# Kernel optimization log

Measured on AMD Instinct MI355X. Metric: run time of the kernel, lower is better.

The kernel has to match this reference:

```python
import jax, jax.numpy as jnp
import numpy as np

B, C, D, H, W = 2, 64, 8, 32, 32
QK = max(1, C // 8)  # intermediate dim for query/key 1x1x1 convs


def setup_inputs() -> dict:
    key = jax.random.key(0)
    ks = jax.random.split(key, 8)
    s = 0.05
    return {
        "x": jax.random.normal(ks[0], (B, C, D, H, W), dtype=jnp.float32),
        "Wq": jax.random.normal(ks[1], (QK, C), dtype=jnp.float32) * s,
        "bq": jax.random.normal(ks[2], (QK,), dtype=jnp.float32) * s,
        "Wk": jax.random.normal(ks[3], (QK, C), dtype=jnp.float32) * s,
        "bk": jax.random.normal(ks[4], (QK,), dtype=jnp.float32) * s,
        "Wv": jax.random.normal(ks[5], (C, C), dtype=jnp.float32) * s,
        "bv": jax.random.normal(ks[6], (C,), dtype=jnp.float32) * s,
        "gamma": jax.random.normal(ks[7], (1,), dtype=jnp.float32) * s,
    }


def reference(x, Wq, bq, Wk, bk, Wv, bv, gamma):
    b, c, d, h, w = x.shape
    n = d * h * w
    xf = x.reshape(b, c, n)  # (B, C, N)
    # 1x1x1 convs == per-position linear maps over channels
    q = jnp.einsum('oc,bcn->bon', Wq, xf) + bq[None, :, None]  # (B, QK, N)
    k = jnp.einsum('oc,bcn->bon', Wk, xf) + bk[None, :, None]  # (B, QK, N)
    v = jnp.einsum('oc,bcn->bon', Wv, xf) + bv[None, :, None]  # (B, C,  N)
    # energy[b, i, j] = q[b, :, i] . k[b, :, j]
    energy = jnp.einsum('bqi,bqj->bij', q, k)  # (B, N, N)
    attn = jax.nn.softmax(energy, axis=-1)
    # out[b, c, i] = sum_j v[b, c, j] * attn[b, i, j]
    out = jnp.einsum('bcj,bij->bci', v, attn)  # (B, C, N)
    out = out.reshape(b, c, d, h, w)
    return gamma[0] * out + x
```

## Files before the change

kernel.cpp:

```cpp
#include <hip/hip_runtime.h>


using f32x16 = __attribute__((ext_vector_type(16))) float;
using u32x4  = __attribute__((ext_vector_type(4))) unsigned int;

#define LOG2E 1.4426950408889634f

static __device__ __forceinline__ f32x16 mfma_z(u32x4 a, u32x4 b) {
  f32x16 d;
  asm("v_mfma_f32_32x32x16_bf16 %0, %1, %2, 0" : "=v"(d) : "v"(a), "v"(b));
  return d;
}
static __device__ __forceinline__ void mfma_acc(f32x16& d, u32x4 a, u32x4 b) {
  asm("v_mfma_f32_32x32x16_bf16 %0, %1, %2, %0" : "+v"(d) : "v"(a), "v"(b));
}
static __device__ __forceinline__ unsigned pkbf(float lo, float hi) {
  unsigned r;
  asm("v_cvt_pk_bf16_f32 %0, %1, %2" : "=v"(r) : "v"(lo), "v"(hi));
  return r;
}
static __device__ __forceinline__ void plswap(unsigned& a, unsigned& b) {
  asm("v_permlane32_swap_b32 %0, %1" : "+v"(a), "+v"(b));
}
static __device__ __forceinline__ unsigned f2bf(float f) {
  union { float f; unsigned u; } v; v.f = f;
  return (v.u + 0x7fffu + ((v.u >> 16) & 1u)) >> 16;
}
static __device__ __forceinline__ u32x4 pack8(const float* p) {
  u32x4 r;
  r[0] = f2bf(p[0]) | (f2bf(p[1]) << 16);
  r[1] = f2bf(p[2]) | (f2bf(p[3]) << 16);
  r[2] = f2bf(p[4]) | (f2bf(p[5]) << 16);
  r[3] = f2bf(p[6]) | (f2bf(p[7]) << 16);
  return r;
}

__global__ __launch_bounds__(128) void k_proj_qk(
    const float* __restrict__ x, const float* __restrict__ Wq, const float* __restrict__ bq,
    const float* __restrict__ Wk, const float* __restrict__ bk,
    u32x4* __restrict__ Qf, u32x4* __restrict__ Kf) {
  __shared__ float sW[2][8][64];
  __shared__ float sb[2][8];
  const int tid = threadIdx.x;
  {
    float* w = &sW[0][0][0];
    for (int i = tid; i < 512; i += 128) { w[i] = Wq[i]; w[512 + i] = Wk[i]; }
    if (tid < 8) { sb[0][tid] = bq[tid]; sb[1][tid] = bk[tid]; }
  }
  __syncthreads();
  const int b    = blockIdx.x >> 7;
  const int nb   = blockIdx.x & 127;
  const int lane = tid & 63;
  const int wv   = tid >> 6;
  const int ql   = lane & 31, ch = lane >> 5;
  const int n    = nb * 64 + wv * 32 + ql;
  const float* xp = x + ((size_t)b << 19) + n;
  float aq[8], ak[8];
  #pragma unroll
  for (int o = 0; o < 8; ++o) { aq[o] = 0.f; ak[o] = 0.f; }
  #pragma unroll
  for (int ci = 0; ci < 32; ci += 4) {
    const int c = ch * 32 + ci;
    float xv[4];
    #pragma unroll
    for (int j = 0; j < 4; ++j) xv[j] = xp[(size_t)(c + j) << 13];
    #pragma unroll
    for (int o = 0; o < 8; ++o) {
      const float4 wq = *(const float4*)&sW[0][o][c];
      const float4 wk = *(const float4*)&sW[1][o][c];
      aq[o] += wq.x * xv[0] + wq.y * xv[1] + wq.z * xv[2] + wq.w * xv[3];
      ak[o] += wk.x * xv[0] + wk.y * xv[1] + wk.z * xv[2] + wk.w * xv[3];
    }
  }
  #pragma unroll
  for (int o = 0; o < 8; ++o) {
    aq[o] += __shfl_xor(aq[o], 32, 64);
    ak[o] += __shfl_xor(ak[o], 32, 64);
  }
  if (ch == 0) {
    float q8[8], k8[8];
    #pragma unroll
    for (int o = 0; o < 8; ++o) {
      q8[o] = (aq[o] + sb[0][o]) * LOG2E;
      k8[o] = ak[o] + sb[1][o];
    }
    Qf[((size_t)b << 13) + n] = pack8(q8);
    Kf[((size_t)b << 13) + n] = pack8(k8);
  }
}

__global__ __launch_bounds__(128) void k_proj_v(
    const float* __restrict__ x, const float* __restrict__ Wv, const float* __restrict__ bv,
    u32x4* __restrict__ Vf) {
  const int bid = blockIdx.x;
  const int b   = bid >> 7;
  const int coq = (bid >> 3) & 15;
  const int ngc = bid & 7;
  const int ng  = ngc * 128 + threadIdx.x;
  const int co  = coq * 4;
  float acc[4][8];
  #pragma unroll
  for (int i = 0; i < 4; ++i)
    #pragma unroll
    for (int e = 0; e < 8; ++e) acc[i][e] = 0.f;
  const float* xb = x + ((size_t)b << 19) + ((size_t)ng << 3);
  for (int c = 0; c < 64; ++c) {
    const float4* xp = (const float4*)(xb + ((size_t)c << 13));
    const float4 x0 = xp[0];
    const float4 x1 = xp[1];
    #pragma unroll
    for (int i = 0; i < 4; ++i) {
      const float wv = Wv[(co + i) * 64 + c];
      acc[i][0] += wv * x0.x; acc[i][1] += wv * x0.y;
      acc[i][2] += wv * x0.z; acc[i][3] += wv * x0.w;
      acc[i][4] += wv * x1.x; acc[i][5] += wv * x1.y;
      acc[i][6] += wv * x1.z; acc[i][7] += wv * x1.w;
    }
  }
  #pragma unroll
  for (int i = 0; i < 4; ++i) {
    const int c = co + i;
    const float bias = bv[c];
    float v8[8];
    #pragma unroll
    for (int e = 0; e < 8; ++e) v8[e] = acc[i][e] + bias;
    const int idx = ((b * 512 + (ng >> 1)) * 2 + (c >> 5)) * 64 + (ng & 1) * 32 + (c & 31);
    Vf[idx] = pack8(v8);
  }
}

__global__ __launch_bounds__(512, 2) void k_attn(
    const u32x4* __restrict__ Qf, const u32x4* __restrict__ Kf, const u32x4* __restrict__ Vf,
    const float* __restrict__ x, const float* __restrict__ gamma, float* __restrict__ out) {
  __shared__ float sO[64 * 64];
  __shared__ float sl[64];
  const int tid  = threadIdx.x;
  const int b    = blockIdx.x >> 7;
  const int qb   = blockIdx.x & 127;
  const int i0   = qb * 64;
  const int w    = tid >> 6;
  const int lane = tid & 63;
  const int ql   = lane & 31;
  const int h    = lane >> 5;

  for (int i = tid; i < 64 * 64; i += 512) sO[i] = 0.f;
  if (tid < 64) sl[tid] = 0.f;
  __syncthreads();

  u32x4 zer; zer[0] = 0u; zer[1] = 0u; zer[2] = 0u; zer[3] = 0u;
  const int qkbase = b * 8192;
  const u32x4 qf0 = (lane < 32) ? Qf[qkbase + i0 + lane] : zer;
  const u32x4 qf1 = (lane < 32) ? Qf[qkbase + i0 + 32 + lane] : zer;

  f32x16 accO[2][2];
  #pragma unroll
  for (int t = 0; t < 2; ++t)
    #pragma unroll
    for (int ct = 0; ct < 2; ++ct)
      #pragma unroll
      for (int r = 0; r < 16; ++r) accO[t][ct][r] = 0.f;
  float lacc[2] = {0.f, 0.f};

  #pragma unroll 2
  for (int it = 0; it < 32; ++it) {
    const int j0 = w * 1024 + it * 32;
    const u32x4 kf = (lane < 32) ? Kf[qkbase + j0 + lane] : zer;
    u32x4 vf[2][2];
    #pragma unroll
    for (int s = 0; s < 2; ++s)
      #pragma unroll
      for (int ct = 0; ct < 2; ++ct)
        vf[s][ct] = Vf[((b * 512 + (j0 >> 4) + s) * 2 + ct) * 64 + lane];

    #pragma unroll
    for (int t = 0; t < 2; ++t) {
      const u32x4 qf = t ? qf1 : qf0;
      f32x16 sacc = mfma_z(kf, qf);
      float p[16];
      #pragma unroll
      for (int r = 0; r < 16; ++r) p[r] = __builtin_exp2f(sacc[r]);
      lacc[t] += (((p[0] + p[1]) + (p[2] + p[3])) + ((p[4] + p[5]) + (p[6] + p[7])))
               + (((p[8] + p[9]) + (p[10] + p[11])) + ((p[12] + p[13]) + (p[14] + p[15])));
      unsigned wd[4][2];
      #pragma unroll
      for (int qq = 0; qq < 4; ++qq) {
        wd[qq][0] = pkbf(p[4 * qq + 0], p[4 * qq + 1]);
        wd[qq][1] = pkbf(p[4 * qq + 2], p[4 * qq + 3]);
      }
      plswap(wd[0][0], wd[1][0]);
      plswap(wd[0][1], wd[1][1]);
      plswap(wd[2][0], wd[3][0]);
      plswap(wd[2][1], wd[3][1]);
      u32x4 pf0, pf1;
      pf0[0] = wd[0][0]; pf0[1] = wd[0][1]; pf0[2] = wd[1][0]; pf0[3] = wd[1][1];
      pf1[0] = wd[2][0]; pf1[1] = wd[2][1]; pf1[2] = wd[3][0]; pf1[3] = wd[3][1];
      #pragma unroll
      for (int ct = 0; ct < 2; ++ct) {
        mfma_acc(accO[t][ct], vf[0][ct], pf0);
        mfma_acc(accO[t][ct], vf[1][ct], pf1);
      }
    }
  }

  #pragma unroll
  for (int t = 0; t < 2; ++t) {
    #pragma unroll
    for (int ct = 0; ct < 2; ++ct)
      #pragma unroll
      for (int r = 0; r < 16; ++r) {
        const int crow = ct * 32 + (r & 3) + 8 * (r >> 2) + 4 * h;
        atomicAdd(&sO[crow * 64 + t * 32 + ql], accO[t][ct][r]);
      }
    atomicAdd(&sl[t * 32 + ql], lacc[t]);
  }
  __syncthreads();

  const float g  = gamma[0];
  const int   c  = tid >> 3;
  const int   qg = (tid & 7) * 8;
  const size_t base = (((size_t)b * 64 + c) << 13) + i0 + qg;
  #pragma unroll
  for (int e = 0; e < 8; ++e) {
    const float ov = sO[c * 64 + qg + e] / sl[qg + e];
    out[base + e] = g * ov + x[base + e];
  }
}

extern "C" void kernel_launch(void* const* d_in, const int* in_sizes, int n_in,
                              void* d_out, int out_size, void* d_ws, size_t ws_size,
                              hipStream_t stream) {
  const float* x  = (const float*)d_in[0];
  const float* Wq = (const float*)d_in[1];
  const float* bq = (const float*)d_in[2];
  const float* Wk = (const float*)d_in[3];
  const float* bk = (const float*)d_in[4];
  const float* Wv = (const float*)d_in[5];
  const float* bv = (const float*)d_in[6];
  const float* gm = (const float*)d_in[7];
  if (ws_size < 2621440u) return;
  char* ws = (char*)d_ws;
  u32x4* Qf = (u32x4*)(ws);
  u32x4* Kf = (u32x4*)(ws + (256 << 10));
  u32x4* Vf = (u32x4*)(ws + (512 << 10));
  float* out = (float*)d_out;

  k_proj_qk<<<dim3(256), dim3(128), 0, stream>>>(x, Wq, bq, Wk, bk, Qf, Kf);
  k_proj_v <<<dim3(256), dim3(128), 0, stream>>>(x, Wv, bv, Vf);
  k_attn   <<<dim3(256), dim3(512), 0, stream>>>(Qf, Kf, Vf, x, gm, out);
}
```

Before: 97.74 us.

## Merge projection kernels and split attention into 32-query blocks with prefetch

The QK and V projection kernels are merged into one launch of 768 blocks, with the V part now computing 2 output channels per block instead of 4. The attention kernel handles 32 queries per block instead of 64, which doubles the grid to 512 blocks and raises the occupancy hint to 4 blocks per CU. Its inner loop is restructured into a manually double-buffered K/V prefetch. It also pads the shared reduction buffer to avoid bank conflicts and vectorizes the epilogue with float4. The goal is to fill the GPU with more blocks and hide load latency, at the cost of each block reusing K/V loads across fewer queries.

```diff
diff --git a/kernel.cpp b/kernel.cpp
--- a/kernel.cpp
+++ b/kernel.cpp
@@ -35,195 +35,193 @@
   return r;
 }
 
-__global__ __launch_bounds__(128) void k_proj_qk(
-    const float* __restrict__ x, const float* __restrict__ Wq, const float* __restrict__ bq,
+__global__ __launch_bounds__(128) void k_proj(
+    const float* __restrict__ x,
+    const float* __restrict__ Wq, const float* __restrict__ bq,
     const float* __restrict__ Wk, const float* __restrict__ bk,
-    u32x4* __restrict__ Qf, u32x4* __restrict__ Kf) {
+    const float* __restrict__ Wv, const float* __restrict__ bv,
+    u32x4* __restrict__ Qf, u32x4* __restrict__ Kf, u32x4* __restrict__ Vf) {
   __shared__ float sW[2][8][64];
   __shared__ float sb[2][8];
   const int tid = threadIdx.x;
-  {
-    float* w = &sW[0][0][0];
-    for (int i = tid; i < 512; i += 128) { w[i] = Wq[i]; w[512 + i] = Wk[i]; }
-    if (tid < 8) { sb[0][tid] = bq[tid]; sb[1][tid] = bk[tid]; }
+  if (blockIdx.x < 256) {
+    {
+      float* wp = &sW[0][0][0];
+      for (int i = tid; i < 512; i += 128) { wp[i] = Wq[i]; wp[512 + i] = Wk[i]; }
+      if (tid < 8) { sb[0][tid] = bq[tid]; sb[1][tid] = bk[tid]; }
+    }
+    __syncthreads();
+    const int b    = blockIdx.x >> 7;
+    const int nb   = blockIdx.x & 127;
+    const int lane = tid & 63;
+    const int wv   = tid >> 6;
+    const int ql   = lane & 31, ch = lane >> 5;
+    const int n    = nb * 64 + wv * 32 + ql;
+    const float* xp = x + ((size_t)b << 19) + n;
+    float aq[8], ak[8];
+    #pragma unroll
+    for (int o = 0; o < 8; ++o) { aq[o] = 0.f; ak[o] = 0.f; }
+    #pragma unroll
+    for (int ci = 0; ci < 32; ci += 4) {
+      const int c = ch * 32 + ci;
+      float xv[4];
+      #pragma unroll
+      for (int j = 0; j < 4; ++j) xv[j] = xp[(size_t)(c + j) << 13];
+      #pragma unroll
+      for (int o = 0; o < 8; ++o) {
+        const float4 wq = *(const float4*)&sW[0][o][c];
+        const float4 wk = *(const float4*)&sW[1][o][c];
+        aq[o] += wq.x * xv[0] + wq.y * xv[1] + wq.z * xv[2] + wq.w * xv[3];
+        ak[o] += wk.x * xv[0] + wk.y * xv[1] + wk.z * xv[2] + wk.w * xv[3];
+      }
+    }
+    #pragma unroll
+    for (int o = 0; o < 8; ++o) {
+      aq[o] += __shfl_xor(aq[o], 32, 64);
+      ak[o] += __shfl_xor(ak[o], 32, 64);
+    }
+    if (ch == 0) {
+      float q8[8], k8[8];
+      #pragma unroll
+      for (int o = 0; o < 8; ++o) {
+        q8[o] = (aq[o] + sb[0][o]) * LOG2E;
+        k8[o] = ak[o] + sb[1][o];
+      }
+      Qf[((size_t)b << 13) + n] = pack8(q8);
+      Kf[((size_t)b << 13) + n] = pack8(k8);
+    }
+  } else {
+    const int bid = blockIdx.x - 256;
+    const int b   = bid >> 8;
+    const int coq = (bid >> 3) & 31;
+    const int ngc = bid & 7;
+    const int ng  = ngc * 128 + tid;
+    const int co  = coq * 2;
+    float acc[2][8];
+    #pragma unroll
+    for (int i = 0; i < 2; ++i)
+      #pragma unroll
+      for (int e = 0; e < 8; ++e) acc[i][e] = 0.f;
+    const float* xb = x + ((size_t)b << 19) + ((size_t)ng << 3);
+    for (int c = 0; c < 64; ++c) {
+      const float4* xp = (const float4*)(xb + ((size_t)c << 13));
+      const float4 x0 = xp[0];
+      const float4 x1 = xp[1];
+      #pragma unroll
+      for (int i = 0; i < 2; ++i) {
+        const float wv = Wv[(co + i) * 64 + c];
+        acc[i][0] += wv * x0.x; acc[i][1] += wv * x0.y;
+        acc[i][2] += wv * x0.z; acc[i][3] += wv * x0.w;
+        acc[i][4] += wv * x1.x; acc[i][5] += wv * x1.y;
+        acc[i][6] += wv * x1.z; acc[i][7] += wv * x1.w;
+      }
+    }
+    #pragma unroll
+    for (int i = 0; i < 2; ++i) {
+      const int c = co + i;
+      const float bias = bv[c];
+      float v8[8];
+      #pragma unroll
+      for (int e = 0; e < 8; ++e) v8[e] = acc[i][e] + bias;
+      const int idx = ((b * 512 + (ng >> 1)) * 2 + (c >> 5)) * 64 + (ng & 1) * 32 + (c & 31);
+      Vf[idx] = pack8(v8);
+    }
   }
-  __syncthreads();
-  const int b    = blockIdx.x >> 7;
-  const int nb   = blockIdx.x & 127;
-  const int lane = tid & 63;
-  const int wv   = tid >> 6;
-  const int ql   = lane & 31, ch = lane >> 5;
-  const int n    = nb * 64 + wv * 32 + ql;
-  const float* xp = x + ((size_t)b << 19) + n;
-  float aq[8], ak[8];
-  #pragma unroll
-  for (int o = 0; o < 8; ++o) { aq[o] = 0.f; ak[o] = 0.f; }
-  #pragma unroll
-  for (int ci = 0; ci < 32; ci += 4) {
-    const int c = ch * 32 + ci;
-    float xv[4];
-    #pragma unroll
-    for (int j = 0; j < 4; ++j) xv[j] = xp[(size_t)(c + j) << 13];
-    #pragma unroll
-    for (int o = 0; o < 8; ++o) {
-      const float4 wq = *(const float4*)&sW[0][o][c];
-      const float4 wk = *(const float4*)&sW[1][o][c];
-      aq[o] += wq.x * xv[0] + wq.y * xv[1] + wq.z * xv[2] + wq.w * xv[3];
-      ak[o] += wk.x * xv[0] + wk.y * xv[1] + wk.z * xv[2] + wk.w * xv[3];
-    }
-  }
-  #pragma unroll
-  for (int o = 0; o < 8; ++o) {
-    aq[o] += __shfl_xor(aq[o], 32, 64);
-    ak[o] += __shfl_xor(ak[o], 32, 64);
-  }
-  if (ch == 0) {
-    float q8[8], k8[8];
-    #pragma unroll
-    for (int o = 0; o < 8; ++o) {
-      q8[o] = (aq[o] + sb[0][o]) * LOG2E;
-      k8[o] = ak[o] + sb[1][o];
-    }
-    Qf[((size_t)b << 13) + n] = pack8(q8);
-    Kf[((size_t)b << 13) + n] = pack8(k8);
-  }
-}
-
-__global__ __launch_bounds__(128) void k_proj_v(
-    const float* __restrict__ x, const float* __restrict__ Wv, const float* __restrict__ bv,
-    u32x4* __restrict__ Vf) {
-  const int bid = blockIdx.x;
-  const int b   = bid >> 7;
-  const int coq = (bid >> 3) & 15;
-  const int ngc = bid & 7;
-  const int ng  = ngc * 128 + threadIdx.x;
-  const int co  = coq * 4;
-  float acc[4][8];
-  #pragma unroll
-  for (int i = 0; i < 4; ++i)
-    #pragma unroll
-    for (int e = 0; e < 8; ++e) acc[i][e] = 0.f;
-  const float* xb = x + ((size_t)b << 19) + ((size_t)ng << 3);
-  for (int c = 0; c < 64; ++c) {
-    const float4* xp = (const float4*)(xb + ((size_t)c << 13));
-    const float4 x0 = xp[0];
-    const float4 x1 = xp[1];
-    #pragma unroll
-    for (int i = 0; i < 4; ++i) {
-      const float wv = Wv[(co + i) * 64 + c];
-      acc[i][0] += wv * x0.x; acc[i][1] += wv * x0.y;
-      acc[i][2] += wv * x0.z; acc[i][3] += wv * x0.w;
-      acc[i][4] += wv * x1.x; acc[i][5] += wv * x1.y;
-      acc[i][6] += wv * x1.z; acc[i][7] += wv * x1.w;
-    }
-  }
-  #pragma unroll
-  for (int i = 0; i < 4; ++i) {
-    const int c = co + i;
-    const float bias = bv[c];
-    float v8[8];
-    #pragma unroll
-    for (int e = 0; e < 8; ++e) v8[e] = acc[i][e] + bias;
-    const int idx = ((b * 512 + (ng >> 1)) * 2 + (c >> 5)) * 64 + (ng & 1) * 32 + (c & 31);
-    Vf[idx] = pack8(v8);
-  }
-}
-
-__global__ __launch_bounds__(512, 2) void k_attn(
+}
+
+__global__ __launch_bounds__(512, 4) void k_attn(
     const u32x4* __restrict__ Qf, const u32x4* __restrict__ Kf, const u32x4* __restrict__ Vf,
     const float* __restrict__ x, const float* __restrict__ gamma, float* __restrict__ out) {
-  __shared__ float sO[64 * 64];
-  __shared__ float sl[64];
+  __shared__ float sO[64][33];
+  __shared__ float sl[32];
   const int tid  = threadIdx.x;
-  const int b    = blockIdx.x >> 7;
-  const int qb   = blockIdx.x & 127;
-  const int i0   = qb * 64;
+  const int b    = blockIdx.x >> 8;
+  const int qb   = blockIdx.x & 255;
+  const int i0   = qb * 32;
   const int w    = tid >> 6;
   const int lane = tid & 63;
   const int ql   = lane & 31;
   const int h    = lane >> 5;
 
-  for (int i = tid; i < 64 * 64; i += 512) sO[i] = 0.f;
-  if (tid < 64) sl[tid] = 0.f;
+  for (int i = tid; i < 64 * 33; i += 512) (&sO[0][0])[i] = 0.f;
+  if (tid < 32) sl[tid] = 0.f;
   __syncthreads();
 
   u32x4 zer; zer[0] = 0u; zer[1] = 0u; zer[2] = 0u; zer[3] = 0u;
   const int qkbase = b * 8192;
-  const u32x4 qf0 = (lane < 32) ? Qf[qkbase + i0 + lane] : zer;
-  const u32x4 qf1 = (lane < 32) ? Qf[qkbase + i0 + 32 + lane] : zer;
-
-  f32x16 accO[2][2];
+  const u32x4 qf = (lane < 32) ? Qf[qkbase + i0 + lane] : zer;
+
+  f32x16 acc0, acc1;
   #pragma unroll
-  for (int t = 0; t < 2; ++t)
-    #pragma unroll
-    for (int ct = 0; ct < 2; ++ct)
-      #pragma unroll
-      for (int r = 0; r < 16; ++r) accO[t][ct][r] = 0.f;
-  float lacc[2] = {0.f, 0.f};
-
-  #pragma unroll 2
-  for (int it = 0; it < 32; ++it) {
-    const int j0 = w * 1024 + it * 32;
-    const u32x4 kf = (lane < 32) ? Kf[qkbase + j0 + lane] : zer;
-    u32x4 vf[2][2];
-    #pragma unroll
-    for (int s = 0; s < 2; ++s)
-      #pragma unroll
-      for (int ct = 0; ct < 2; ++ct)
-        vf[s][ct] = Vf[((b * 512 + (j0 >> 4) + s) * 2 + ct) * 64 + lane];
-
-    #pragma unroll
-    for (int t = 0; t < 2; ++t) {
-      const u32x4 qf = t ? qf1 : qf0;
-      f32x16 sacc = mfma_z(kf, qf);
-      float p[16];
-      #pragma unroll
-      for (int r = 0; r < 16; ++r) p[r] = __builtin_exp2f(sacc[r]);
-      lacc[t] += (((p[0] + p[1]) + (p[2] + p[3])) + ((p[4] + p[5]) + (p[6] + p[7])))
-               + (((p[8] + p[9]) + (p[10] + p[11])) + ((p[12] + p[13]) + (p[14] + p[15])));
-      unsigned wd[4][2];
-      #pragma unroll
-      for (int qq = 0; qq < 4; ++qq) {
-        wd[qq][0] = pkbf(p[4 * qq + 0], p[4 * qq + 1]);
-        wd[qq][1] = pkbf(p[4 * qq + 2], p[4 * qq + 3]);
-      }
-      plswap(wd[0][0], wd[1][0]);
-      plswap(wd[0][1], wd[1][1]);
-      plswap(wd[2][0], wd[3][0]);
-      plswap(wd[2][1], wd[3][1]);
-      u32x4 pf0, pf1;
-      pf0[0] = wd[0][0]; pf0[1] = wd[0][1]; pf0[2] = wd[1][0]; pf0[3] = wd[1][1];
-      pf1[0] = wd[2][0]; pf1[1] = wd[2][1]; pf1[2] = wd[3][0]; pf1[3] = wd[3][1];
-      #pragma unroll
-      for (int ct = 0; ct < 2; ++ct) {
-        mfma_acc(accO[t][ct], vf[0][ct], pf0);
-        mfma_acc(accO[t][ct], vf[1][ct], pf1);
-      }
-    }
+  for (int r = 0; r < 16; ++r) { acc0[r] = 0.f; acc1[r] = 0.f; }
+  float lacc = 0.f;
+
+  const int jbase = qkbase + w * 1024;
+  const u32x4* __restrict__ vbase = Vf + ((size_t)(b * 512 + w * 64) << 7) + lane;
+
+  auto body = [&](const u32x4& kf, const u32x4* vf) {
+    f32x16 sacc = mfma_z(kf, qf);
+    float p[16];
+    #pragma unroll
+    for (int r = 0; r < 16; ++r) p[r] = __builtin_exp2f(sacc[r]);
+    lacc += (((p[0] + p[1]) + (p[2] + p[3])) + ((p[4] + p[5]) + (p[6] + p[7])))
+          + (((p[8] + p[9]) + (p[10] + p[11])) + ((p[12] + p[13]) + (p[14] + p[15])));
+    unsigned wd[4][2];
+    #pragma unroll
+    for (int qq = 0; qq < 4; ++qq) {
+      wd[qq][0] = pkbf(p[4 * qq + 0], p[4 * qq + 1]);
+      wd[qq][1] = pkbf(p[4 * qq + 2], p[4 * qq + 3]);
+    }
+    plswap(wd[0][0], wd[1][0]);
+    plswap(wd[0][1], wd[1][1]);
+    plswap(wd[2][0], wd[3][0]);
+    plswap(wd[2][1], wd[3][1]);
+    u32x4 pf0, pf1;
+    pf0[0] = wd[0][0]; pf0[1] = wd[0][1]; pf0[2] = wd[1][0]; pf0[3] = wd[1][1];
+    pf1[0] = wd[2][0]; pf1[1] = wd[2][1]; pf1[2] = wd[3][0]; pf1[3] = wd[3][1];
+    mfma_acc(acc0, vf[0], pf0);
+    mfma_acc(acc1, vf[1], pf0);
+    mfma_acc(acc0, vf[2], pf1);
+    mfma_acc(acc1, vf[3], pf1);
+  };
+
+  u32x4 kA, kB, vA[4], vB[4];
+  kA = (lane < 32) ? Kf[jbase + lane] : zer;
+  { const u32x4* vp = vbase;
+    vA[0] = vp[0]; vA[1] = vp[64]; vA[2] = vp[128]; vA[3] = vp[192]; }
+  #pragma unroll 1
+  for (int it = 0; it < 32; it += 2) {
+    kB = (lane < 32) ? Kf[jbase + (it + 1) * 32 + lane] : zer;
+    { const u32x4* vp = vbase + (size_t)(it + 1) * 256;
+      vB[0] = vp[0]; vB[1] = vp[64]; vB[2] = vp[128]; vB[3] = vp[192]; }
+    body(kA, vA);
+    const int n2 = (it + 2) & 31;
+    kA = (lane < 32) ? Kf[jbase + n2 * 32 + lane] : zer;
+    { const u32x4* vp = vbase + (size_t)n2 * 256;
+      vA[0] = vp[0]; vA[1] = vp[64]; vA[2] = vp[128]; vA[3] = vp[192]; }
+    body(kB, vB);
   }
 
   #pragma unroll
-  for (int t = 0; t < 2; ++t) {
-    #pragma unroll
-    for (int ct = 0; ct < 2; ++ct)
-      #pragma unroll
-      for (int r = 0; r < 16; ++r) {
-        const int crow = ct * 32 + (r & 3) + 8 * (r >> 2) + 4 * h;
-        atomicAdd(&sO[crow * 64 + t * 32 + ql], accO[t][ct][r]);
-      }
-    atomicAdd(&sl[t * 32 + ql], lacc[t]);
+  for (int r = 0; r < 16; ++r) {
+    const int cr = (r & 3) + 8 * (r >> 2) + 4 * h;
+    atomicAdd(&sO[cr][ql], acc0[r]);
+    atomicAdd(&sO[cr + 32][ql], acc1[r]);
   }
+  atomicAdd(&sl[ql], lacc);
   __syncthreads();
 
   const float g  = gamma[0];
   const int   c  = tid >> 3;
-  const int   qg = (tid & 7) * 8;
+  const int   qg = (tid & 7) * 4;
   const size_t base = (((size_t)b * 64 + c) << 13) + i0 + qg;
-  #pragma unroll
-  for (int e = 0; e < 8; ++e) {
-    const float ov = sO[c * 64 + qg + e] / sl[qg + e];
-    out[base + e] = g * ov + x[base + e];
-  }
+  const float4 xv = *(const float4*)&x[base];
+  float4 o;
+  o.x = g * (sO[c][qg + 0] / sl[qg + 0]) + xv.x;
+  o.y = g * (sO[c][qg + 1] / sl[qg + 1]) + xv.y;
+  o.z = g * (sO[c][qg + 2] / sl[qg + 2]) + xv.z;
+  o.w = g * (sO[c][qg + 3] / sl[qg + 3]) + xv.w;
+  *(float4*)&out[base] = o;
 }
 
 extern "C" void kernel_launch(void* const* d_in, const int* in_sizes, int n_in,
@@ -244,7 +242,6 @@
   u32x4* Vf = (u32x4*)(ws + (512 << 10));
   float* out = (float*)d_out;
 
-  k_proj_qk<<<dim3(256), dim3(128), 0, stream>>>(x, Wq, bq, Wk, bk, Qf, Kf);
-  k_proj_v <<<dim3(256), dim3(128), 0, stream>>>(x, Wv, bv, Vf);
-  k_attn   <<<dim3(256), dim3(512), 0, stream>>>(Qf, Kf, Vf, x, gm, out);
-}
+  k_proj<<<dim3(768), dim3(128), 0, stream>>>(x, Wq, bq, Wk, bk, Wv, bv, Qf, Kf, Vf);
+  k_attn<<<dim3(512), dim3(512), 0, stream>>>(Qf, Kf, Vf, x, gm, out);
+}
```

After: 79.15 us. 19.0% less time.
